# Performance work log

Hardware: AMD Instinct MI355X
Metric: run time of the kernel (lower is better)

The kernel has to match this reference:

```python
import jax, jax.numpy as jnp
import numpy as np

B, SQ, SK, D, N, H = 2, 2048, 2048, 1024, 16, 64
EPS = 1e-5


def setup_inputs() -> dict:
    key = jax.random.key(0)
    ks = jax.random.split(key, 8)
    inv_d = 1.0 / np.sqrt(D)
    inv_h = 1.0 / np.sqrt(H)
    # causal mask: True = masked (filled with -inf), matching torch.where(mask, IGNORE, attn)
    mask = jnp.triu(jnp.ones((SQ, SK), dtype=bool), k=1)
    return {
        "x_q": jax.random.normal(ks[0], (B, SQ, D), dtype=jnp.float32),
        "x_kv": jax.random.normal(ks[1], (B, SK, D), dtype=jnp.float32),
        "mask": mask,
        "W_Q": jax.random.normal(ks[2], (N, D, H), dtype=jnp.float32) * inv_d,
        "W_K": jax.random.normal(ks[3], (N, D, H), dtype=jnp.float32) * inv_d,
        "W_V": jax.random.normal(ks[4], (N, D, H), dtype=jnp.float32) * inv_d,
        "W_O": jax.random.normal(ks[5], (N, H, D), dtype=jnp.float32) * inv_h,
        "b_Q": jnp.zeros((N, H), dtype=jnp.float32),
        "b_K": jnp.zeros((N, H), dtype=jnp.float32),
        "b_V": jnp.zeros((N, H), dtype=jnp.float32),
        "b_O": jnp.zeros((D,), dtype=jnp.float32),
        "ln1_g": jnp.ones((H,), dtype=jnp.float32),
        "ln1_b": jnp.zeros((H,), dtype=jnp.float32),
        "ln2_g": jnp.ones((H,), dtype=jnp.float32),
        "ln2_b": jnp.zeros((H,), dtype=jnp.float32),
    }


def _layernorm(x, g, b):
    # LayerNorm over last dim (d_head), eps=1e-5, biased variance (torch default)
    m = jnp.mean(x, axis=-1, keepdims=True)
    v = jnp.mean(jnp.square(x - m), axis=-1, keepdims=True)
    return (x - m) * jax.lax.rsqrt(v + EPS) * g + b


def reference(x_q, x_kv, mask, W_Q, W_K, W_V, W_O, b_Q, b_K, b_V, b_O,
              ln1_g, ln1_b, ln2_g, ln2_b):
    q = jnp.einsum('bsd,ndh->bsnh', x_q, W_Q) + b_Q    # [B,SQ,N,H]
    k = jnp.einsum('bsd,ndh->bsnh', x_kv, W_K) + b_K   # [B,SK,N,H]
    v = jnp.einsum('bsd,ndh->bsnh', x_kv, W_V) + b_V   # [B,SK,N,H]
    q = _layernorm(q, ln1_g, ln1_b)
    k = _layernorm(k, ln2_g, ln2_b)
    # NOTE: no 1/sqrt(d_head) scaling, faithful to the source module
    attn = jnp.einsum('bqnh,bknh->bnqk', q, k)         # [B,N,SQ,SK]
    attn = jnp.where(mask, -jnp.inf, attn)
    probas = jax.nn.softmax(attn, axis=-1)
    z = jnp.einsum('bnqk,bknh->bqnh', probas, v)       # [B,SQ,N,H]
    out = jnp.einsum('bqnh,nhd->bqd', z, W_O) + b_O    # [B,SQ,D]
    return (out, k, v)
```

## Files before the change

kernel.cpp:

```cpp
#include <hip/hip_runtime.h>
#include <math.h>

namespace {
constexpr int kB  = 2;
constexpr int kS  = 2048;
constexpr int kD  = 1024;
constexpr int kN  = 16;
constexpr int kH  = 64;
constexpr int kBS = kB * kS;
constexpr int kNH = kN * kH;
}

typedef __bf16 bf16x4 __attribute__((ext_vector_type(4)));
typedef __bf16 bf16x8 __attribute__((ext_vector_type(8)));
typedef float  f32x4  __attribute__((ext_vector_type(4)));
typedef unsigned int u32x4 __attribute__((ext_vector_type(4)));

__device__ inline unsigned pkbf(float a, float b) {
  unsigned short ua = __builtin_bit_cast(unsigned short, (__bf16)a);
  unsigned short ub = __builtin_bit_cast(unsigned short, (__bf16)b);
  return (unsigned)ua | ((unsigned)ub << 16);
}

__global__ __launch_bounds__(256) void prep_all(
    const float* __restrict__ xq, const float* __restrict__ xkv,
    const float* __restrict__ WQ, const float* __restrict__ WK,
    const float* __restrict__ WV, const float* __restrict__ WO,
    __bf16* __restrict__ xqH, __bf16* __restrict__ xqL,
    __bf16* __restrict__ xkH, __bf16* __restrict__ xkL,
    __bf16* __restrict__ QH, __bf16* __restrict__ QL,
    __bf16* __restrict__ KHo, __bf16* __restrict__ KLo,
    __bf16* __restrict__ VH,
    __bf16* __restrict__ WOtH)
{
  const int bx = blockIdx.x;
  const int t = threadIdx.x;
  __shared__ float T[64][65];

  if (bx < 8192) {
    const float* in;
    __bf16 *oH, *oL;
    long long i4;
    if (bx < 4096) { in = xq;  oH = xqH; oL = xqL; i4 = (long long)bx * 256 + t; }
    else           { in = xkv; oH = xkH; oL = xkL; i4 = (long long)(bx - 4096) * 256 + t; }
    const float4 v = *(const float4*)(in + i4 * 4);
    const float x[4] = {v.x, v.y, v.z, v.w};
    bf16x4 hi, lo;
#pragma unroll
    for (int i = 0; i < 4; ++i) {
      const __bf16 h = (__bf16)x[i];
      hi[i] = h;
      lo[i] = (__bf16)(x[i] - (float)h);
    }
    *(bf16x4*)(oH + i4 * 4) = hi;
    *(bf16x4*)(oL + i4 * 4) = lo;
    return;
  }

  if (bx < 8960) {
    const int zz = bx - 8192;
    const int bxx = zz & 15;
    const int z   = zz >> 4;
    const int which = z >> 4;
    const bool wantLo = (which < 2);
    const float* __restrict__ in = (which == 0) ? WQ : (which == 1) ? WK : WV;
    __bf16* __restrict__ oH = (which == 0) ? QH : (which == 1) ? KHo : VH;
    __bf16* __restrict__ oL = (which == 0) ? QL : KLo;
    const int head = z & 15;
    const long long inB  = (long long)head * 65536 + (long long)(bxx * 64) * 64;
    const long long outB = (long long)head * 65536 + bxx * 64;
#pragma unroll
    for (int rr = 0; rr < 4; ++rr) {
      const int i = rr * 16 + (t >> 4);
      const int j = (t & 15) * 4;
      const float4 v = *(const float4*)(in + inB + (long long)i * 64 + j);
      T[i][j + 0] = v.x; T[i][j + 1] = v.y; T[i][j + 2] = v.z; T[i][j + 3] = v.w;
    }
    __syncthreads();
#pragma unroll
    for (int rr = 0; rr < 4; ++rr) {
      const int hh = rr * 16 + (t >> 4);
      const int kk = (t & 15) * 4;
      bf16x4 hi, lo;
#pragma unroll
      for (int m = 0; m < 4; ++m) {
        const float x = T[kk + m][hh];
        const __bf16 h = (__bf16)x;
        hi[m] = h;
        lo[m] = (__bf16)(x - (float)h);
      }
      *(bf16x4*)(oH + outB + (long long)hh * 1024 + kk) = hi;
      if (wantLo)
        *(bf16x4*)(oL + outB + (long long)hh * 1024 + kk) = lo;
    }
    return;
  }

  {
    const int zz = bx - 8960;
    const int bxx = zz & 15;
    const int byy = zz >> 4;
    const long long inB  = (long long)(bxx * 64) * 1024 + byy * 64;
    const long long outB = (long long)(byy * 64) * 1024 + bxx * 64;
#pragma unroll
    for (int rr = 0; rr < 4; ++rr) {
      const int i = rr * 16 + (t >> 4);
      const int j = (t & 15) * 4;
      const float4 v = *(const float4*)(WO + inB + (long long)i * 1024 + j);
      T[i][j + 0] = v.x; T[i][j + 1] = v.y; T[i][j + 2] = v.z; T[i][j + 3] = v.w;
    }
    __syncthreads();
#pragma unroll
    for (int rr = 0; rr < 4; ++rr) {
      const int hh = rr * 16 + (t >> 4);
      const int kk = (t & 15) * 4;
      bf16x4 hi;
#pragma unroll
      for (int m = 0; m < 4; ++m) hi[m] = (__bf16)T[kk + m][hh];
      *(bf16x4*)(WOtH + outB + (long long)hh * 1024 + kk) = hi;
    }
  }
}

__global__ __launch_bounds__(256) void qkv_gemm128v(
    const __bf16* __restrict__ xqH, const __bf16* __restrict__ xqL,
    const __bf16* __restrict__ xkH, const __bf16* __restrict__ xkL,
    const __bf16* __restrict__ WQH, const __bf16* __restrict__ WQL,
    const __bf16* __restrict__ WKH, const __bf16* __restrict__ WKL,
    const __bf16* __restrict__ WVH,
    const float* __restrict__ b_Q, const float* __restrict__ b_K,
    const float* __restrict__ b_V,
    const float* __restrict__ ln1g, const float* __restrict__ ln1b,
    const float* __restrict__ ln2g, const float* __restrict__ ln2b,
    float* __restrict__ out_k, float* __restrict__ out_v,
    __bf16* __restrict__ qH, __bf16* __restrict__ qL,
    __bf16* __restrict__ kHp, __bf16* __restrict__ kLp,
    __bf16* __restrict__ vT)
{
  const int mode = blockIdx.z;
  const int row0 = blockIdx.x * 128;
  const int ct   = blockIdx.y;
  const bool split = (mode < 2);

  __shared__ __align__(16) char SM[36864];
  char* const ABuf = SM;
  char* const BBuf = SM + 16384;

  const int t = threadIdx.x;
  const int lane = t & 63;
  const int w = t >> 6;
  const int l16 = lane & 15;
  const int quad = lane >> 4;
  const int mBase = (w & 1) * 64;
  const int nBase = (w >> 1) * 64;

  const __bf16* __restrict__ aHp = (mode == 0) ? xqH : xkH;
  const __bf16* __restrict__ aLq = split ? ((mode == 0) ? xqL : xkL) : aHp;
  const __bf16* __restrict__ bHp = (mode == 0) ? WQH : (mode == 1) ? WKH : WVH;
  const __bf16* __restrict__ bLq = split ? ((mode == 0) ? WQL : WKL) : bHp;

  f32x4 acc[4][4] = {};

  const int srow8 = lane >> 3;
  const int p     = lane & 7;
  const int sw2l  = (srow8 & 1) | ((srow8 & 2) << 1) | ((srow8 & 4) >> 1);
  const int u     = p ^ sw2l;
  const int ucol  = (u & 3) * 8;
  const __bf16* __restrict__ pA = (u < 4) ? aHp : aLq;
  const __bf16* __restrict__ pB = (u < 4) ? bHp : bLq;
  const long long gA0 = (long long)(row0 + w * 32 + srow8) * 1024 + ucol;
  const long long gB0 = (long long)(ct * 128 + w * 32 + srow8) * 1024 + ucol;
  char* const ABufW = ABuf + w * 4096;
  char* const BBufW = BBuf + w * 4096;

  const int r8  = l16 & 7;
  const int rs2 = (r8 & 1) | ((r8 & 2) << 1) | ((r8 & 4) >> 1);
  const int rof = (quad ^ rs2) << 4;

  auto COMPUTE = [&]() {
    bf16x8 ah[4], bh[4];
#pragma unroll
    for (int mt = 0; mt < 4; ++mt)
      ah[mt] = *(const bf16x8*)(ABuf + (mBase + mt * 16 + l16) * 128 + rof);
#pragma unroll
    for (int nt = 0; nt < 4; ++nt)
      bh[nt] = *(const bf16x8*)(BBuf + (nBase + nt * 16 + l16) * 128 + rof);
#pragma unroll
    for (int mt = 0; mt < 4; ++mt)
#pragma unroll
      for (int nt = 0; nt < 4; ++nt)
        acc[mt][nt] = __builtin_amdgcn_mfma_f32_16x16x32_bf16(ah[mt], bh[nt], acc[mt][nt], 0, 0, 0);
    if (split) {
      bf16x8 bl[4];
#pragma unroll
      for (int nt = 0; nt < 4; ++nt)
        bl[nt] = *(const bf16x8*)(BBuf + (nBase + nt * 16 + l16) * 128 + (rof ^ 64));
#pragma unroll
      for (int mt = 0; mt < 4; ++mt)
#pragma unroll
        for (int nt = 0; nt < 4; ++nt)
          acc[mt][nt] = __builtin_amdgcn_mfma_f32_16x16x32_bf16(ah[mt], bl[nt], acc[mt][nt], 0, 0, 0);
      bf16x8 al[4];
#pragma unroll
      for (int mt = 0; mt < 4; ++mt)
        al[mt] = *(const bf16x8*)(ABuf + (mBase + mt * 16 + l16) * 128 + (rof ^ 64));
#pragma unroll
      for (int mt = 0; mt < 4; ++mt)
#pragma unroll
        for (int nt = 0; nt < 4; ++nt)
          acc[mt][nt] = __builtin_amdgcn_mfma_f32_16x16x32_bf16(al[mt], bh[nt], acc[mt][nt], 0, 0, 0);
    }
  };

  for (int k0 = 0; k0 < 1024; k0 += 32) {
    if (k0) __syncthreads();
#pragma unroll
    for (int i = 0; i < 4; ++i) {
      __builtin_amdgcn_global_load_lds(
          (const __attribute__((address_space(1))) void*)(pA + gA0 + (long long)i * 8192 + k0),
          (__attribute__((address_space(3))) void*)(ABufW + i * 1024), 16, 0, 0);
      __builtin_amdgcn_global_load_lds(
          (const __attribute__((address_space(1))) void*)(pB + gB0 + (long long)i * 8192 + k0),
          (__attribute__((address_space(3))) void*)(BBufW + i * 1024), 16, 0, 0);
    }
    __syncthreads();
    COMPUTE();
  }

  const float* __restrict__ bias = (mode == 0) ? b_Q : (mode == 1) ? b_K : b_V;
  float bi[4];
#pragma unroll
  for (int nt = 0; nt < 4; ++nt) bi[nt] = bias[ct * 128 + nBase + nt * 16 + l16];

  if (mode <= 1) {
    const float* __restrict__ lg = (mode == 0) ? ln1g : ln2g;
    const float* __restrict__ lb = (mode == 0) ? ln1b : ln2b;
    float gg[4], bb[4];
#pragma unroll
    for (int nt = 0; nt < 4; ++nt) {
      gg[nt] = lg[nt * 16 + l16];
      bb[nt] = lb[nt * 16 + l16];
    }
#pragma unroll
    for (int mt = 0; mt < 4; ++mt)
#pragma unroll
      for (int r4 = 0; r4 < 4; ++r4) {
        float y[4];
#pragma unroll
        for (int nt = 0; nt < 4; ++nt) y[nt] = acc[mt][nt][r4] + bi[nt];
        float s = y[0] + y[1] + y[2] + y[3];
#pragma unroll
        for (int o = 8; o >= 1; o >>= 1) s += __shfl_xor(s, o);
        const float m = s * (1.0f / 64.0f);
        float vs = 0.0f;
#pragma unroll
        for (int nt = 0; nt < 4; ++nt) {
          const float d = y[nt] - m;
          vs += d * d;
        }
#pragma unroll
        for (int o = 8; o >= 1; o >>= 1) vs += __shfl_xor(vs, o);
        const float inv = rsqrtf(vs * (1.0f / 64.0f) + 1e-5f);
#pragma unroll
        for (int nt = 0; nt < 4; ++nt)
          acc[mt][nt][r4] = (y[nt] - m) * inv * gg[nt] + bb[nt];
      }
  } else {
#pragma unroll
    for (int mt = 0; mt < 4; ++mt)
#pragma unroll
      for (int nt = 0; nt < 4; ++nt)
#pragma unroll
        for (int r4 = 0; r4 < 4; ++r4) acc[mt][nt][r4] += bi[nt];
  }

#pragma unroll
  for (int mt = 0; mt < 4; ++mt)
#pragma unroll
    for (int r4 = 0; r4 < 4; ++r4) {
      const long long row = row0 + mBase + mt * 16 + quad * 4 + r4;
      const long long cb = row * 1024 + ct * 128 + nBase;
      if (mode == 0) {
#pragma unroll
        for (int nt = 0; nt < 4; ++nt) {
          const float x = acc[mt][nt][r4];
          const __bf16 h = (__bf16)x;
          qH[cb + nt * 16 + l16] = h;
          qL[cb + nt * 16 + l16] = (__bf16)(x - (float)h);
        }
      } else if (mode == 1) {
#pragma unroll
        for (int nt = 0; nt < 4; ++nt) {
          const float x = acc[mt][nt][r4];
          out_k[cb + nt * 16 + l16] = x;
          const __bf16 h = (__bf16)x;
          kHp[cb + nt * 16 + l16] = h;
          kLp[cb + nt * 16 + l16] = (__bf16)(x - (float)h);
        }
      } else {
#pragma unroll
        for (int nt = 0; nt < 4; ++nt)
          out_v[cb + nt * 16 + l16] = acc[mt][nt][r4];
      }
    }

  if (mode == 2) {
    __syncthreads();
    __bf16* TT = (__bf16*)SM + w * 4608;
#pragma unroll
    for (int mt = 0; mt < 4; ++mt)
#pragma unroll
      for (int nt = 0; nt < 4; ++nt)
#pragma unroll
        for (int r4 = 0; r4 < 4; ++r4)
          TT[(nt * 16 + l16) * 72 + mt * 16 + quad * 4 + r4] = (__bf16)acc[mt][nt][r4];
    __syncthreads();
    const int b = row0 >> 11;
    const int s0 = (row0 + mBase) & 2047;
    const int head = ct * 2 + (w >> 1);
#pragma unroll
    for (int rep = 0; rep < 8; ++rep) {
      const int h = rep * 8 + (lane >> 3);
      const int s8v = (lane & 7) * 8;
      const bf16x8 vv = *(const bf16x8*)&TT[h * 72 + s8v];
      const int a  = s8v >> 4;
      const int c0 = 32 * (a >> 1) + 8 * ((s8v >> 2) & 3) + 4 * (a & 1);
      __bf16* dst = vT + ((long long)((b * 16 + head) * 64 + h)) * 2048 + s0 + c0;
      const bf16x4 lo = __builtin_shufflevector(vv, vv, 0, 1, 2, 3);
      const bf16x4 hi = __builtin_shufflevector(vv, vv, 4, 5, 6, 7);
      *(bf16x4*)(dst)     = lo;
      *(bf16x4*)(dst + 8) = hi;
    }
  }
}

__global__ __launch_bounds__(256) void ogemm64p(
    const __bf16* __restrict__ zH, const __bf16* __restrict__ WOt,
    const float* __restrict__ b_O, float* __restrict__ out)
{
  const int row0 = blockIdx.x * 64;
  const int ct = blockIdx.y;
  __shared__ __align__(16) __bf16 AS2[2][64][40];
  __shared__ __align__(16) __bf16 BS2[2][128][40];
  const int t = threadIdx.x;
  const int lane = t & 63;
  const int w = t >> 6;
  const int l16 = lane & 15;
  const int quad = lane >> 4;
  const int nBase = w * 32;

  f32x4 acc[4][2] = {};
  const int arow = t >> 2, akh = (t & 3) * 8;
  const int brow = t >> 1, bkh = (t & 1) * 16;

  bf16x8 r0, r1, r2;
  auto loadT = [&](int k0) {
    r0 = *(const bf16x8*)(zH + (long long)(row0 + arow) * 1024 + k0 + akh);
    const long long gb = (long long)(ct * 128 + brow) * 1024 + k0 + bkh;
    r1 = *(const bf16x8*)(WOt + gb);
    r2 = *(const bf16x8*)(WOt + gb + 8);
  };
  loadT(0);
  *(bf16x8*)&AS2[0][arow][akh]     = r0;
  *(bf16x8*)&BS2[0][brow][bkh]     = r1;
  *(bf16x8*)&BS2[0][brow][bkh + 8] = r2;
  __syncthreads();

  for (int k0 = 0; k0 < 1024; k0 += 32) {
    const int cb = (k0 >> 5) & 1;
    const bool more = (k0 + 32 < 1024);
    if (more) loadT(k0 + 32);

    bf16x8 ah[4], bh[2];
#pragma unroll
    for (int mt = 0; mt < 4; ++mt)
      ah[mt] = *(const bf16x8*)&AS2[cb][mt * 16 + l16][quad * 8];
#pragma unroll
    for (int nt = 0; nt < 2; ++nt)
      bh[nt] = *(const bf16x8*)&BS2[cb][nBase + nt * 16 + l16][quad * 8];
#pragma unroll
    for (int mt = 0; mt < 4; ++mt)
#pragma unroll
      for (int nt = 0; nt < 2; ++nt)
        acc[mt][nt] = __builtin_amdgcn_mfma_f32_16x16x32_bf16(ah[mt], bh[nt], acc[mt][nt], 0, 0, 0);

    if (more) {
      const int nb = 1 - cb;
      *(bf16x8*)&AS2[nb][arow][akh]     = r0;
      *(bf16x8*)&BS2[nb][brow][bkh]     = r1;
      *(bf16x8*)&BS2[nb][brow][bkh + 8] = r2;
    }
    __syncthreads();
  }

#pragma unroll
  for (int mt = 0; mt < 4; ++mt)
#pragma unroll
    for (int r4 = 0; r4 < 4; ++r4) {
      const long long row = row0 + mt * 16 + quad * 4 + r4;
#pragma unroll
      for (int nt = 0; nt < 2; ++nt) {
        const int col = ct * 128 + nBase + nt * 16 + l16;
        out[row * 1024 + col] = acc[mt][nt][r4] + b_O[col];
      }
    }
}

__global__ __launch_bounds__(256, 2) void attn_mfma6(
    const __bf16* __restrict__ qHg, const __bf16* __restrict__ qLg,
    const __bf16* __restrict__ kHg, const __bf16* __restrict__ kLg,
    const __bf16* __restrict__ vTg,
    __bf16* __restrict__ zH)
{
  const int p = blockIdx.x;
  const int n = blockIdx.y;
  const int b = blockIdx.z;

  __shared__ __align__(16) char SM[49152];

  const int t = threadIdx.x;
  const int lane = t & 63;
  const int w = t >> 6;
  const int l16 = lane & 15;
  const int quad = lane >> 4;
  const int skey = t >> 2;
  const int sh16 = (t & 3) * 16;
  const int su   = sh16 >> 3;
  const int sx   = (skey & 7) << 4;
  const int rx   = (l16 & 7) << 4;

  bf16x8 rk0, rk1, rl0, rl1, rv0, rv1;
  auto storeKV = [&](int buf) {
    char* base = SM + buf * 8192 + skey * 128;
    *(bf16x8*)(base +         (((su    ) << 4) ^ sx)) = rk0;
    *(bf16x8*)(base +         (((su + 1) << 4) ^ sx)) = rk1;
    *(bf16x8*)(base + 16384 + (((su    ) << 4) ^ sx)) = rl0;
    *(bf16x8*)(base + 16384 + (((su + 1) << 4) ^ sx)) = rl1;
    *(bf16x8*)(base + 32768 + (((su    ) << 4) ^ sx)) = rv0;
    *(bf16x8*)(base + 32768 + (((su + 1) << 4) ^ sx)) = rv1;
  };

  for (int half = 0; half < 2; ++half) {
    const int qt = half ? p : (31 - p);
    const int q0 = qt * 64;

    bf16x8 Qh[2], Ql[2];
    {
      const long long qrow = (long long)(b * kS + q0 + w * 16 + l16) * 1024 + n * 64 + quad * 8;
      Qh[0] = *(const bf16x8*)(qHg + qrow);
      Qh[1] = *(const bf16x8*)(qHg + qrow + 32);
      Ql[0] = *(const bf16x8*)(qLg + qrow);
      Ql[1] = *(const bf16x8*)(qLg + qrow + 32);
    }

    f32x4 O[4] = {};
    float mrun = -3.0e38f, lrun = 0.0f;
    const int qg = q0 + w * 16 + l16;

    auto loadKV = [&](int k0) {
      const long long gk = (long long)(b * kS + k0 + skey) * 1024 + n * 64 + sh16;
      rk0 = *(const bf16x8*)(kHg + gk);
      rk1 = *(const bf16x8*)(kHg + gk + 8);
      rl0 = *(const bf16x8*)(kLg + gk);
      rl1 = *(const bf16x8*)(kLg + gk + 8);
      const long long gv = ((long long)(b * kN + n) * 64 + skey) * 2048 + k0 + sh16;
      rv0 = *(const bf16x8*)(vTg + gv);
      rv1 = *(const bf16x8*)(vTg + gv + 8);
    };

    loadKV(0);
    storeKV(0);
    __syncthreads();

    for (int kt = 0; kt <= qt; ++kt) {
      const int cb = kt & 1;
      const bool more = (kt < qt);
      if (more) loadKV((kt + 1) * 64);

      const char* KHb = SM + cb * 8192;
      const char* KLb = KHb + 16384;
      const char* VSb = KHb + 32768;

      f32x4 S[4] = {};
      __builtin_amdgcn_s_setprio(1);
#pragma unroll
      for (int kc = 0; kc < 4; ++kc) {
        const int ro = (kc * 16 + l16) * 128;
        const bf16x8 kh0 = *(const bf16x8*)(KHb + ro + (((quad    ) << 4) ^ rx));
        const bf16x8 kh1 = *(const bf16x8*)(KHb + ro + (((quad + 4) << 4) ^ rx));
        const bf16x8 kl0 = *(const bf16x8*)(KLb + ro + (((quad    ) << 4) ^ rx));
        const bf16x8 kl1 = *(const bf16x8*)(KLb + ro + (((quad + 4) << 4) ^ rx));
        S[kc] = __builtin_amdgcn_mfma_f32_16x16x32_bf16(kh0, Qh[0], S[kc], 0, 0, 0);
        S[kc] = __builtin_amdgcn_mfma_f32_16x16x32_bf16(kh1, Qh[1], S[kc], 0, 0, 0);
        S[kc] = __builtin_amdgcn_mfma_f32_16x16x32_bf16(kl0, Qh[0], S[kc], 0, 0, 0);
        S[kc] = __builtin_amdgcn_mfma_f32_16x16x32_bf16(kl1, Qh[1], S[kc], 0, 0, 0);
        S[kc] = __builtin_amdgcn_mfma_f32_16x16x32_bf16(kh0, Ql[0], S[kc], 0, 0, 0);
        S[kc] = __builtin_amdgcn_mfma_f32_16x16x32_bf16(kh1, Ql[1], S[kc], 0, 0, 0);
      }
      __builtin_amdgcn_s_setprio(0);

      if (kt == qt) {
#pragma unroll
        for (int kc = 0; kc < 4; ++kc) {
          const int key = q0 + kc * 16 + quad * 4;
#pragma unroll
          for (int r = 0; r < 4; ++r)
            if (key + r > qg) S[kc][r] = -3.0e38f;
        }
      }

      float pm = fmaxf(fmaxf(S[0][0], S[0][1]), fmaxf(S[0][2], S[0][3]));
      pm = fmaxf(pm, fmaxf(fmaxf(S[1][0], S[1][1]), fmaxf(S[1][2], S[1][3])));
      pm = fmaxf(pm, fmaxf(fmaxf(S[2][0], S[2][1]), fmaxf(S[2][2], S[2][3])));
      pm = fmaxf(pm, fmaxf(fmaxf(S[3][0], S[3][1]), fmaxf(S[3][2], S[3][3])));
      pm = fmaxf(pm, __shfl_xor(pm, 16));
      pm = fmaxf(pm, __shfl_xor(pm, 32));

      const bool upd = __any(pm > mrun + 8.0f);
      const float mref = upd ? fmaxf(mrun, pm) : mrun;
      float ls = 0.0f;
#pragma unroll
      for (int kc = 0; kc < 4; ++kc)
#pragma unroll
        for (int r = 0; r < 4; ++r) {
          const float pe = __expf(S[kc][r] - mref);
          S[kc][r] = pe;
          ls += pe;
        }
      ls += __shfl_xor(ls, 16);
      ls += __shfl_xor(ls, 32);

      if (upd) {
        const float alpha = __expf(mrun - mref);
        lrun = lrun * alpha + ls;
        float aB[4];
#pragma unroll
        for (int r = 0; r < 4; ++r)
          aB[r] = __shfl(alpha, (lane & 48) | (quad * 4 + r));
#pragma unroll
        for (int hc = 0; hc < 4; ++hc)
#pragma unroll
          for (int r = 0; r < 4; ++r) O[hc][r] *= aB[r];
        mrun = mref;
      } else {
        lrun += ls;
      }

      u32x4 pw0, pw1;
      pw0[0] = pkbf(S[0][0], S[0][1]); pw0[1] = pkbf(S[0][2], S[0][3]);
      pw0[2] = pkbf(S[1][0], S[1][1]); pw0[3] = pkbf(S[1][2], S[1][3]);
      pw1[0] = pkbf(S[2][0], S[2][1]); pw1[1] = pkbf(S[2][2], S[2][3]);
      pw1[2] = pkbf(S[3][0], S[3][1]); pw1[3] = pkbf(S[3][2], S[3][3]);
      const bf16x8 Pa0 = __builtin_bit_cast(bf16x8, pw0);
      const bf16x8 Pa1 = __builtin_bit_cast(bf16x8, pw1);

      __builtin_amdgcn_s_setprio(1);
#pragma unroll
      for (int hc = 0; hc < 4; ++hc) {
        const int ro = (hc * 16 + l16) * 128;
        const bf16x8 vb0 = *(const bf16x8*)(VSb + ro + (((quad    ) << 4) ^ rx));
        const bf16x8 vb1 = *(const bf16x8*)(VSb + ro + (((quad + 4) << 4) ^ rx));
        O[hc] = __builtin_amdgcn_mfma_f32_16x16x32_bf16(Pa0, vb0, O[hc], 0, 0, 0);
        O[hc] = __builtin_amdgcn_mfma_f32_16x16x32_bf16(Pa1, vb1, O[hc], 0, 0, 0);
      }
      __builtin_amdgcn_s_setprio(0);

      if (more) storeKV(1 - cb);
      __syncthreads();
    }

    float linv[4];
#pragma unroll
    for (int r = 0; r < 4; ++r)
      linv[r] = 1.0f / __shfl(lrun, (lane & 48) | (quad * 4 + r));
#pragma unroll
    for (int r = 0; r < 4; ++r) {
      const long long zrow = (long long)(b * kS + q0 + w * 16 + quad * 4 + r) * 1024 + n * 64;
#pragma unroll
      for (int hc = 0; hc < 4; ++hc)
        zH[zrow + hc * 16 + l16] = (__bf16)(O[hc][r] * linv[r]);
    }
  }
}

__global__ __launch_bounds__(256) void sgemm64(
    const float* __restrict__ A, int lda,
    const float* __restrict__ Bbase, long long bStride, int colMul, int ldb,
    float* __restrict__ C, int ldc,
    const float* __restrict__ bias, int K)
{
  const int row0 = blockIdx.x * 64;
  const int ct = blockIdx.y;
  const float* __restrict__ Bp = Bbase + (long long)ct * bStride;
  const int col0B = ct * colMul;
  const int col0C = ct * 64;
  __shared__ float As[16][68];
  __shared__ float Bs[16][68];
  const int t = threadIdx.x;
  const int ty = t >> 4;
  const int tx = t & 15;
  float acc[4][4] = {};
  for (int k0 = 0; k0 < K; k0 += 16) {
    {
      const int r = t >> 2;
      const int kk = (t & 3) * 4;
      const float4 a4 = *(const float4*)(A + (long long)(row0 + r) * lda + k0 + kk);
      As[kk + 0][r] = a4.x; As[kk + 1][r] = a4.y; As[kk + 2][r] = a4.z; As[kk + 3][r] = a4.w;
    }
    {
      const int kk = t >> 4;
      const int c = (t & 15) * 4;
      *(float4*)&Bs[kk][c] = *(const float4*)(Bp + (long long)(k0 + kk) * ldb + col0B + c);
    }
    __syncthreads();
#pragma unroll
    for (int kk = 0; kk < 16; ++kk) {
      const float4 a4 = *(const float4*)&As[kk][ty * 4];
      const float4 b4 = *(const float4*)&Bs[kk][tx * 4];
      const float av[4] = {a4.x, a4.y, a4.z, a4.w};
      const float bv[4] = {b4.x, b4.y, b4.z, b4.w};
#pragma unroll
      for (int i = 0; i < 4; ++i)
#pragma unroll
        for (int j = 0; j < 4; ++j)
          acc[i][j] = fmaf(av[i], bv[j], acc[i][j]);
    }
    __syncthreads();
  }
#pragma unroll
  for (int i = 0; i < 4; ++i) {
    const int r = row0 + ty * 4 + i;
    float4 o;
    o.x = acc[i][0] + bias[col0C + tx * 4 + 0];
    o.y = acc[i][1] + bias[col0C + tx * 4 + 1];
    o.z = acc[i][2] + bias[col0C + tx * 4 + 2];
    o.w = acc[i][3] + bias[col0C + tx * 4 + 3];
    *(float4*)(C + (long long)r * ldc + col0C + tx * 4) = o;
  }
}

__global__ __launch_bounds__(256) void ln64(
    float* __restrict__ X, const float* __restrict__ g,
    const float* __restrict__ bta, int nrows)
{
  const int row = blockIdx.x * 4 + (threadIdx.x >> 6);
  const int lane = threadIdx.x & 63;
  if (row >= nrows) return;
  const float x = X[(long long)row * 64 + lane];
  float s = x;
#pragma unroll
  for (int o = 32; o >= 1; o >>= 1) s += __shfl_xor(s, o);
  const float m = s * (1.0f / 64.0f);
  const float d = x - m;
  float vs = d * d;
#pragma unroll
  for (int o = 32; o >= 1; o >>= 1) vs += __shfl_xor(vs, o);
  const float inv = rsqrtf(vs * (1.0f / 64.0f) + 1e-5f);
  X[(long long)row * 64 + lane] = d * inv * g[lane] + bta[lane];
}

__global__ __launch_bounds__(256) void attn_mfma(
    const float* __restrict__ Q, const float* __restrict__ Kg,
    const float* __restrict__ Vg, float* __restrict__ Z)
{
  const int qt = (gridDim.x - 1) - blockIdx.x;
  const int n = blockIdx.y;
  const int b = blockIdx.z;
  const int q0 = qt * 64;
  __shared__ __bf16 KH[64][72];
  __shared__ __bf16 KL[64][72];
  __shared__ __bf16 VS[64][72];
  const int t = threadIdx.x;
  const int lane = t & 63;
  const int w = t >> 6;
  const int l16 = lane & 15;
  const int quad = lane >> 4;
  bf16x8 Qh[2], Ql[2];
  {
    const long long qrow = ((long long)(b * kS + q0 + w * 16 + l16)) * kNH + n * kH + quad * 8;
#pragma unroll
    for (int c = 0; c < 2; ++c) {
      const float4 a = *(const float4*)(Q + qrow + c * 32);
      const float4 bq = *(const float4*)(Q + qrow + c * 32 + 4);
      const float x[8] = {a.x, a.y, a.z, a.w, bq.x, bq.y, bq.z, bq.w};
#pragma unroll
      for (int i = 0; i < 8; ++i) {
        const __bf16 h = (__bf16)x[i];
        Qh[c][i] = h;
        Ql[c][i] = (__bf16)(x[i] - (float)h);
      }
    }
  }
  f32x4 O[4] = {};
  float mrow[4] = {-3.0e38f, -3.0e38f, -3.0e38f, -3.0e38f};
  float lrow[4] = {};
  for (int kt = 0; kt <= qt; ++kt) {
    const int k0 = kt * 64;
    __syncthreads();
#pragma unroll
    for (int rep = 0; rep < 4; ++rep) {
      {
        const int row = rep * 16 + (t >> 4);
        const int h4 = (t & 15) * 4;
        const float4 k4 = *(const float4*)(Kg + ((long long)(b * kS + k0 + row)) * kNH + n * kH + h4);
        const float x[4] = {k4.x, k4.y, k4.z, k4.w};
        bf16x4 hi, lo;
#pragma unroll
        for (int i = 0; i < 4; ++i) {
          const __bf16 h = (__bf16)x[i];
          hi[i] = h;
          lo[i] = (__bf16)(x[i] - (float)h);
        }
        *(bf16x4*)&KH[row][h4] = hi;
        *(bf16x4*)&KL[row][h4] = lo;
      }
      {
        const int key = rep * 16 + (t & 15);
        const int h4 = (t >> 4) * 4;
        const float4 v4 = *(const float4*)(Vg + ((long long)(b * kS + k0 + key)) * kNH + n * kH + h4);
        VS[h4 + 0][key] = (__bf16)v4.x;
        VS[h4 + 1][key] = (__bf16)v4.y;
        VS[h4 + 2][key] = (__bf16)v4.z;
        VS[h4 + 3][key] = (__bf16)v4.w;
      }
    }
    __syncthreads();
    f32x4 S[4] = {};
#pragma unroll
    for (int kc = 0; kc < 4; ++kc) {
      const int row = kc * 16 + l16;
      const bf16x8 kh0 = *(const bf16x8*)&KH[row][quad * 8];
      const bf16x8 kh1 = *(const bf16x8*)&KH[row][32 + quad * 8];
      const bf16x8 kl0 = *(const bf16x8*)&KL[row][quad * 8];
      const bf16x8 kl1 = *(const bf16x8*)&KL[row][32 + quad * 8];
      S[kc] = __builtin_amdgcn_mfma_f32_16x16x32_bf16(Qh[0], kh0, S[kc], 0, 0, 0);
      S[kc] = __builtin_amdgcn_mfma_f32_16x16x32_bf16(Qh[1], kh1, S[kc], 0, 0, 0);
      S[kc] = __builtin_amdgcn_mfma_f32_16x16x32_bf16(Qh[0], kl0, S[kc], 0, 0, 0);
      S[kc] = __builtin_amdgcn_mfma_f32_16x16x32_bf16(Qh[1], kl1, S[kc], 0, 0, 0);
      S[kc] = __builtin_amdgcn_mfma_f32_16x16x32_bf16(Ql[0], kh0, S[kc], 0, 0, 0);
      S[kc] = __builtin_amdgcn_mfma_f32_16x16x32_bf16(Ql[1], kh1, S[kc], 0, 0, 0);
    }
    if (kt == qt) {
#pragma unroll
      for (int kc = 0; kc < 4; ++kc) {
        const int key = k0 + kc * 16 + l16;
#pragma unroll
        for (int r = 0; r < 4; ++r) {
          const int q = q0 + w * 16 + quad * 4 + r;
          if (key > q) S[kc][r] = -3.0e38f;
        }
      }
    }
#pragma unroll
    for (int r = 0; r < 4; ++r) {
      float mt = fmaxf(fmaxf(S[0][r], S[1][r]), fmaxf(S[2][r], S[3][r]));
#pragma unroll
      for (int o = 8; o >= 1; o >>= 1) mt = fmaxf(mt, __shfl_xor(mt, o));
      const float mnew = fmaxf(mrow[r], mt);
      const float alpha = __expf(mrow[r] - mnew);
      mrow[r] = mnew;
      float ls = 0.0f;
#pragma unroll
      for (int kc = 0; kc < 4; ++kc) {
        const float pe = __expf(S[kc][r] - mnew);
        S[kc][r] = pe;
        ls += pe;
      }
#pragma unroll
      for (int o = 8; o >= 1; o >>= 1) ls += __shfl_xor(ls, o);
      lrow[r] = lrow[r] * alpha + ls;
#pragma unroll
      for (int hc = 0; hc < 4; ++hc) O[hc][r] *= alpha;
    }
    __syncthreads();
    __bf16(*Ps)[72] = KL;
#pragma unroll
    for (int kc = 0; kc < 4; ++kc)
#pragma unroll
      for (int r = 0; r < 4; ++r)
        Ps[w * 16 + quad * 4 + r][kc * 16 + l16] = (__bf16)S[kc][r];
    bf16x8 Pa[2];
#pragma unroll
    for (int c = 0; c < 2; ++c)
      Pa[c] = *(const bf16x8*)&Ps[w * 16 + l16][c * 32 + quad * 8];
#pragma unroll
    for (int hc = 0; hc < 4; ++hc) {
      const int hrow = hc * 16 + l16;
      const bf16x8 vb0 = *(const bf16x8*)&VS[hrow][quad * 8];
      const bf16x8 vb1 = *(const bf16x8*)&VS[hrow][32 + quad * 8];
      O[hc] = __builtin_amdgcn_mfma_f32_16x16x32_bf16(Pa[0], vb0, O[hc], 0, 0, 0);
      O[hc] = __builtin_amdgcn_mfma_f32_16x16x32_bf16(Pa[1], vb1, O[hc], 0, 0, 0);
    }
  }
#pragma unroll
  for (int r = 0; r < 4; ++r) {
    const float inv = 1.0f / lrow[r];
    const long long zrow = ((long long)(b * kS + q0 + w * 16 + quad * 4 + r)) * kNH + n * kH;
#pragma unroll
    for (int hc = 0; hc < 4; ++hc)
      Z[zrow + hc * 16 + l16] = O[hc][r] * inv;
  }
}

extern "C" void kernel_launch(void* const* d_in, const int* in_sizes, int n_in,
                              void* d_out, int out_size, void* d_ws, size_t ws_size,
                              hipStream_t stream)
{
  const float* x_q   = (const float*)d_in[0];
  const float* x_kv  = (const float*)d_in[1];
  const float* W_Q   = (const float*)d_in[3];
  const float* W_K   = (const float*)d_in[4];
  const float* W_V   = (const float*)d_in[5];
  const float* W_O   = (const float*)d_in[6];
  const float* b_Q   = (const float*)d_in[7];
  const float* b_K   = (const float*)d_in[8];
  const float* b_V   = (const float*)d_in[9];
  const float* b_O   = (const float*)d_in[10];
  const float* ln1_g = (const float*)d_in[11];
  const float* ln1_b = (const float*)d_in[12];
  const float* ln2_g = (const float*)d_in[13];
  const float* ln2_b = (const float*)d_in[14];

  float* out_o = (float*)d_out;
  float* out_k = out_o + 4194304;
  float* out_v = out_o + 8388608;

  const dim3 blk(256);

  if (ws_size >= (72ull << 20)) {
    char* W = (char*)d_ws;
    __bf16* xqH = (__bf16*)(W);
    __bf16* xqL = xqH + 4194304;
    __bf16* xkH = (__bf16*)(W + (16ull << 20));
    __bf16* xkL = xkH + 4194304;
    __bf16* wp  = (__bf16*)(W + (32ull << 20));
    __bf16 *WtQH = wp,            *WtQL = wp + 1048576;
    __bf16 *WtKH = wp + 2097152,  *WtKL = wp + 3145728;
    __bf16 *WtVH = wp + 4194304;
    __bf16 *WOtH = wp + 6291456;
    __bf16* kHp = (__bf16*)(W + (48ull << 20));
    __bf16* kLp = kHp + 4194304;
    __bf16* vT  = (__bf16*)(W + (64ull << 20));
    __bf16* zH = xqH;
    __bf16* qH = (__bf16*)out_o;
    __bf16* qL = qH + 4194304;

    hipLaunchKernelGGL(prep_all, dim3(9216), blk, 0, stream,
                       x_q, x_kv, W_Q, W_K, W_V, W_O,
                       xqH, xqL, xkH, xkL,
                       WtQH, WtQL, WtKH, WtKL, WtVH, WOtH);

    hipLaunchKernelGGL(qkv_gemm128v, dim3(32, 8, 3), blk, 0, stream,
                       xqH, xqL, xkH, xkL,
                       WtQH, WtQL, WtKH, WtKL, WtVH,
                       b_Q, b_K, b_V, ln1_g, ln1_b, ln2_g, ln2_b,
                       out_k, out_v, qH, qL, kHp, kLp, vT);

    hipLaunchKernelGGL(attn_mfma6, dim3(16, 16, 2), blk, 0, stream,
                       qH, qL, kHp, kLp, vT, zH);

    hipLaunchKernelGGL(ogemm64p, dim3(64, 8), blk, 0, stream,
                       zH, WOtH, b_O, out_o);
  } else {
    float* ws_q = out_o;
    float* ws_z = (float*)d_ws;
    const dim3 gproj(kBS / 64, kN);
    hipLaunchKernelGGL(sgemm64, gproj, blk, 0, stream,
                       x_q, kD, W_Q, (long long)kD * kH, 0, kH, ws_q, kNH, b_Q, kD);
    hipLaunchKernelGGL(sgemm64, gproj, blk, 0, stream,
                       x_kv, kD, W_K, (long long)kD * kH, 0, kH, out_k, kNH, b_K, kD);
    hipLaunchKernelGGL(sgemm64, gproj, blk, 0, stream,
                       x_kv, kD, W_V, (long long)kD * kH, 0, kH, out_v, kNH, b_V, kD);
    const int nrows = kBS * kN;
    hipLaunchKernelGGL(ln64, dim3(nrows / 4), blk, 0, stream, ws_q, ln1_g, ln1_b, nrows);
    hipLaunchKernelGGL(ln64, dim3(nrows / 4), blk, 0, stream, out_k, ln2_g, ln2_b, nrows);
    hipLaunchKernelGGL(attn_mfma, dim3(kS / 64, kN, kB), blk, 0, stream,
                       ws_q, out_k, out_v, ws_z);
    hipLaunchKernelGGL(sgemm64, dim3(kBS / 64, kD / 64), blk, 0, stream,
                       ws_z, kNH, W_O, 0LL, 64, kD, out_o, kD, b_O, kD);
  }
}
```

Measured before the change: 295.4 us.

## Enlarge attention query tile to 128 rows with two 16-row slices per wave

The attention kernel now gives each wave two 16-row query slices (128 query rows per block), so every K/V tile staged in shared memory feeds twice as many MFMAs. This halves the total K/V global traffic and shared-memory reads per unit of compute. The grid drops to 8x16x2 blocks with launch bounds of one block per SIMD, so occupancy and parallelism fall and register pressure from the doubled accumulators and softmax state rises. Causal masking now covers the last two key tiles of each query block.

After: 304.5 us. +3.1%, slower.

```diff
diff --git a/kernel.cpp b/kernel.cpp
--- a/kernel.cpp
+++ b/kernel.cpp
@@ -406,7 +406,7 @@
     }
 }
 
-__global__ __launch_bounds__(256, 2) void attn_mfma6(
+__global__ __launch_bounds__(256, 1) void attn_mfma7(
     const __bf16* __restrict__ qHg, const __bf16* __restrict__ qLg,
     const __bf16* __restrict__ kHg, const __bf16* __restrict__ kLg,
     const __bf16* __restrict__ vTg,
@@ -441,21 +441,28 @@
   };
 
   for (int half = 0; half < 2; ++half) {
-    const int qt = half ? p : (31 - p);
-    const int q0 = qt * 64;
-
-    bf16x8 Qh[2], Ql[2];
+    const int qt = half ? p : (15 - p);
+    const int q0 = qt * 128;
+    const int nkt = 2 * qt + 2;
+
+    bf16x8 QhA[2], QlA[2], QhB[2], QlB[2];
     {
-      const long long qrow = (long long)(b * kS + q0 + w * 16 + l16) * 1024 + n * 64 + quad * 8;
-      Qh[0] = *(const bf16x8*)(qHg + qrow);
-      Qh[1] = *(const bf16x8*)(qHg + qrow + 32);
-      Ql[0] = *(const bf16x8*)(qLg + qrow);
-      Ql[1] = *(const bf16x8*)(qLg + qrow + 32);
-    }
-
-    f32x4 O[4] = {};
-    float mrun = -3.0e38f, lrun = 0.0f;
-    const int qg = q0 + w * 16 + l16;
+      const long long qrowA = (long long)(b * kS + q0 + w * 32 + l16) * 1024 + n * 64 + quad * 8;
+      QhA[0] = *(const bf16x8*)(qHg + qrowA);
+      QhA[1] = *(const bf16x8*)(qHg + qrowA + 32);
+      QlA[0] = *(const bf16x8*)(qLg + qrowA);
+      QlA[1] = *(const bf16x8*)(qLg + qrowA + 32);
+      const long long qrowB = qrowA + 16 * 1024;
+      QhB[0] = *(const bf16x8*)(qHg + qrowB);
+      QhB[1] = *(const bf16x8*)(qHg + qrowB + 32);
+      QlB[0] = *(const bf16x8*)(qLg + qrowB);
+      QlB[1] = *(const bf16x8*)(qLg + qrowB + 32);
+    }
+
+    f32x4 OA[4] = {}, OB[4] = {};
+    float mA = -3.0e38f, lA = 0.0f, mB = -3.0e38f, lB = 0.0f;
+    const int qa = q0 + w * 32 + l16;
+    const int qb = qa + 16;
 
     auto loadKV = [&](int k0) {
       const long long gk = (long long)(b * kS + k0 + skey) * 1024 + n * 64 + sh16;
@@ -472,16 +479,16 @@
     storeKV(0);
     __syncthreads();
 
-    for (int kt = 0; kt <= qt; ++kt) {
+    for (int kt = 0; kt < nkt; ++kt) {
       const int cb = kt & 1;
-      const bool more = (kt < qt);
+      const bool more = (kt + 1 < nkt);
       if (more) loadKV((kt + 1) * 64);
 
       const char* KHb = SM + cb * 8192;
       const char* KLb = KHb + 16384;
       const char* VSb = KHb + 32768;
 
-      f32x4 S[4] = {};
+      f32x4 SA[4] = {}, SB[4] = {};
       __builtin_amdgcn_s_setprio(1);
 #pragma unroll
       for (int kc = 0; kc < 4; ++kc) {
@@ -490,69 +497,117 @@
         const bf16x8 kh1 = *(const bf16x8*)(KHb + ro + (((quad + 4) << 4) ^ rx));
         const bf16x8 kl0 = *(const bf16x8*)(KLb + ro + (((quad    ) << 4) ^ rx));
         const bf16x8 kl1 = *(const bf16x8*)(KLb + ro + (((quad + 4) << 4) ^ rx));
-        S[kc] = __builtin_amdgcn_mfma_f32_16x16x32_bf16(kh0, Qh[0], S[kc], 0, 0, 0);
-        S[kc] = __builtin_amdgcn_mfma_f32_16x16x32_bf16(kh1, Qh[1], S[kc], 0, 0, 0);
-        S[kc] = __builtin_amdgcn_mfma_f32_16x16x32_bf16(kl0, Qh[0], S[kc], 0, 0, 0);
-        S[kc] = __builtin_amdgcn_mfma_f32_16x16x32_bf16(kl1, Qh[1], S[kc], 0, 0, 0);
-        S[kc] = __builtin_amdgcn_mfma_f32_16x16x32_bf16(kh0, Ql[0], S[kc], 0, 0, 0);
-        S[kc] = __builtin_amdgcn_mfma_f32_16x16x32_bf16(kh1, Ql[1], S[kc], 0, 0, 0);
+        SA[kc] = __builtin_amdgcn_mfma_f32_16x16x32_bf16(kh0, QhA[0], SA[kc], 0, 0, 0);
+        SA[kc] = __builtin_amdgcn_mfma_f32_16x16x32_bf16(kh1, QhA[1], SA[kc], 0, 0, 0);
+        SA[kc] = __builtin_amdgcn_mfma_f32_16x16x32_bf16(kl0, QhA[0], SA[kc], 0, 0, 0);
+        SA[kc] = __builtin_amdgcn_mfma_f32_16x16x32_bf16(kl1, QhA[1], SA[kc], 0, 0, 0);
+        SA[kc] = __builtin_amdgcn_mfma_f32_16x16x32_bf16(kh0, QlA[0], SA[kc], 0, 0, 0);
+        SA[kc] = __builtin_amdgcn_mfma_f32_16x16x32_bf16(kh1, QlA[1], SA[kc], 0, 0, 0);
+        SB[kc] = __builtin_amdgcn_mfma_f32_16x16x32_bf16(kh0, QhB[0], SB[kc], 0, 0, 0);
+        SB[kc] = __builtin_amdgcn_mfma_f32_16x16x32_bf16(kh1, QhB[1], SB[kc], 0, 0, 0);
+        SB[kc] = __builtin_amdgcn_mfma_f32_16x16x32_bf16(kl0, QhB[0], SB[kc], 0, 0, 0);
+        SB[kc] = __builtin_amdgcn_mfma_f32_16x16x32_bf16(kl1, QhB[1], SB[kc], 0, 0, 0);
+        SB[kc] = __builtin_amdgcn_mfma_f32_16x16x32_bf16(kh0, QlB[0], SB[kc], 0, 0, 0);
+        SB[kc] = __builtin_amdgcn_mfma_f32_16x16x32_bf16(kh1, QlB[1], SB[kc], 0, 0, 0);
       }
       __builtin_amdgcn_s_setprio(0);
 
-      if (kt == qt) {
+      if (kt >= 2 * qt) {
 #pragma unroll
         for (int kc = 0; kc < 4; ++kc) {
-          const int key = q0 + kc * 16 + quad * 4;
-#pragma unroll
-          for (int r = 0; r < 4; ++r)
-            if (key + r > qg) S[kc][r] = -3.0e38f;
+          const int key = kt * 64 + kc * 16 + quad * 4;
+#pragma unroll
+          for (int r = 0; r < 4; ++r) {
+            if (key + r > qa) SA[kc][r] = -3.0e38f;
+            if (key + r > qb) SB[kc][r] = -3.0e38f;
+          }
         }
       }
 
-      float pm = fmaxf(fmaxf(S[0][0], S[0][1]), fmaxf(S[0][2], S[0][3]));
-      pm = fmaxf(pm, fmaxf(fmaxf(S[1][0], S[1][1]), fmaxf(S[1][2], S[1][3])));
-      pm = fmaxf(pm, fmaxf(fmaxf(S[2][0], S[2][1]), fmaxf(S[2][2], S[2][3])));
-      pm = fmaxf(pm, fmaxf(fmaxf(S[3][0], S[3][1]), fmaxf(S[3][2], S[3][3])));
-      pm = fmaxf(pm, __shfl_xor(pm, 16));
-      pm = fmaxf(pm, __shfl_xor(pm, 32));
-
-      const bool upd = __any(pm > mrun + 8.0f);
-      const float mref = upd ? fmaxf(mrun, pm) : mrun;
-      float ls = 0.0f;
+      float pmA = fmaxf(fmaxf(SA[0][0], SA[0][1]), fmaxf(SA[0][2], SA[0][3]));
+      pmA = fmaxf(pmA, fmaxf(fmaxf(SA[1][0], SA[1][1]), fmaxf(SA[1][2], SA[1][3])));
+      pmA = fmaxf(pmA, fmaxf(fmaxf(SA[2][0], SA[2][1]), fmaxf(SA[2][2], SA[2][3])));
+      pmA = fmaxf(pmA, fmaxf(fmaxf(SA[3][0], SA[3][1]), fmaxf(SA[3][2], SA[3][3])));
+      pmA = fmaxf(pmA, __shfl_xor(pmA, 16));
+      pmA = fmaxf(pmA, __shfl_xor(pmA, 32));
+      float pmB = fmaxf(fmaxf(SB[0][0], SB[0][1]), fmaxf(SB[0][2], SB[0][3]));
+      pmB = fmaxf(pmB, fmaxf(fmaxf(SB[1][0], SB[1][1]), fmaxf(SB[1][2], SB[1][3])));
+      pmB = fmaxf(pmB, fmaxf(fmaxf(SB[2][0], SB[2][1]), fmaxf(SB[2][2], SB[2][3])));
+      pmB = fmaxf(pmB, fmaxf(fmaxf(SB[3][0], SB[3][1]), fmaxf(SB[3][2], SB[3][3])));
+      pmB = fmaxf(pmB, __shfl_xor(pmB, 16));
+      pmB = fmaxf(pmB, __shfl_xor(pmB, 32));
+
+      const bool updA = __any(pmA > mA + 8.0f);
+      const float mrefA = updA ? fmaxf(mA, pmA) : mA;
+      float lsA = 0.0f;
 #pragma unroll
       for (int kc = 0; kc < 4; ++kc)
 #pragma unroll
         for (int r = 0; r < 4; ++r) {
-          const float pe = __expf(S[kc][r] - mref);
-          S[kc][r] = pe;
-          ls += pe;
+          const float pe = __expf(SA[kc][r] - mrefA);
+          SA[kc][r] = pe;
+          lsA += pe;
         }
-      ls += __shfl_xor(ls, 16);
-      ls += __shfl_xor(ls, 32);
-
-      if (upd) {
-        const float alpha = __expf(mrun - mref);
-        lrun = lrun * alpha + ls;
-        float aB[4];
+      lsA += __shfl_xor(lsA, 16);
+      lsA += __shfl_xor(lsA, 32);
+      if (updA) {
+        const float alpha = __expf(mA - mrefA);
+        lA = lA * alpha + lsA;
+        float aB4[4];
 #pragma unroll
         for (int r = 0; r < 4; ++r)
-          aB[r] = __shfl(alpha, (lane & 48) | (quad * 4 + r));
+          aB4[r] = __shfl(alpha, (lane & 48) | (quad * 4 + r));
 #pragma unroll
         for (int hc = 0; hc < 4; ++hc)
 #pragma unroll
-          for (int r = 0; r < 4; ++r) O[hc][r] *= aB[r];
-        mrun = mref;
+          for (int r = 0; r < 4; ++r) OA[hc][r] *= aB4[r];
+        mA = mrefA;
       } else {
-        lrun += ls;
+        lA += lsA;
+      }
+
+      const bool updB = __any(pmB > mB + 8.0f);
+      const float mrefB = updB ? fmaxf(mB, pmB) : mB;
+      float lsB = 0.0f;
+#pragma unroll
+      for (int kc = 0; kc < 4; ++kc)
+#pragma unroll
+        for (int r = 0; r < 4; ++r) {
+          const float pe = __expf(SB[kc][r] - mrefB);
+          SB[kc][r] = pe;
+          lsB += pe;
+        }
+      lsB += __shfl_xor(lsB, 16);
+      lsB += __shfl_xor(lsB, 32);
+      if (updB) {
+        const float alpha = __expf(mB - mrefB);
+        lB = lB * alpha + lsB;
+        float aB4[4];
+#pragma unroll
+        for (int r = 0; r < 4; ++r)
+          aB4[r] = __shfl(alpha, (lane & 48) | (quad * 4 + r));
+#pragma unroll
+        for (int hc = 0; hc < 4; ++hc)
+#pragma unroll
+          for (int r = 0; r < 4; ++r) OB[hc][r] *= aB4[r];
+        mB = mrefB;
+      } else {
+        lB += lsB;
       }
 
       u32x4 pw0, pw1;
-      pw0[0] = pkbf(S[0][0], S[0][1]); pw0[1] = pkbf(S[0][2], S[0][3]);
-      pw0[2] = pkbf(S[1][0], S[1][1]); pw0[3] = pkbf(S[1][2], S[1][3]);
-      pw1[0] = pkbf(S[2][0], S[2][1]); pw1[1] = pkbf(S[2][2], S[2][3]);
-      pw1[2] = pkbf(S[3][0], S[3][1]); pw1[3] = pkbf(S[3][2], S[3][3]);
-      const bf16x8 Pa0 = __builtin_bit_cast(bf16x8, pw0);
-      const bf16x8 Pa1 = __builtin_bit_cast(bf16x8, pw1);
+      pw0[0] = pkbf(SA[0][0], SA[0][1]); pw0[1] = pkbf(SA[0][2], SA[0][3]);
+      pw0[2] = pkbf(SA[1][0], SA[1][1]); pw0[3] = pkbf(SA[1][2], SA[1][3]);
+      pw1[0] = pkbf(SA[2][0], SA[2][1]); pw1[1] = pkbf(SA[2][2], SA[2][3]);
+      pw1[2] = pkbf(SA[3][0], SA[3][1]); pw1[3] = pkbf(SA[3][2], SA[3][3]);
+      const bf16x8 Pa0A = __builtin_bit_cast(bf16x8, pw0);
+      const bf16x8 Pa1A = __builtin_bit_cast(bf16x8, pw1);
+      pw0[0] = pkbf(SB[0][0], SB[0][1]); pw0[1] = pkbf(SB[0][2], SB[0][3]);
+      pw0[2] = pkbf(SB[1][0], SB[1][1]); pw0[3] = pkbf(SB[1][2], SB[1][3]);
+      pw1[0] = pkbf(SB[2][0], SB[2][1]); pw1[1] = pkbf(SB[2][2], SB[2][3]);
+      pw1[2] = pkbf(SB[3][0], SB[3][1]); pw1[3] = pkbf(SB[3][2], SB[3][3]);
+      const bf16x8 Pa0B = __builtin_bit_cast(bf16x8, pw0);
+      const bf16x8 Pa1B = __builtin_bit_cast(bf16x8, pw1);
 
       __builtin_amdgcn_s_setprio(1);
 #pragma unroll
@@ -560,8 +615,10 @@
         const int ro = (hc * 16 + l16) * 128;
         const bf16x8 vb0 = *(const bf16x8*)(VSb + ro + (((quad    ) << 4) ^ rx));
         const bf16x8 vb1 = *(const bf16x8*)(VSb + ro + (((quad + 4) << 4) ^ rx));
-        O[hc] = __builtin_amdgcn_mfma_f32_16x16x32_bf16(Pa0, vb0, O[hc], 0, 0, 0);
-        O[hc] = __builtin_amdgcn_mfma_f32_16x16x32_bf16(Pa1, vb1, O[hc], 0, 0, 0);
+        OA[hc] = __builtin_amdgcn_mfma_f32_16x16x32_bf16(Pa0A, vb0, OA[hc], 0, 0, 0);
+        OA[hc] = __builtin_amdgcn_mfma_f32_16x16x32_bf16(Pa1A, vb1, OA[hc], 0, 0, 0);
+        OB[hc] = __builtin_amdgcn_mfma_f32_16x16x32_bf16(Pa0B, vb0, OB[hc], 0, 0, 0);
+        OB[hc] = __builtin_amdgcn_mfma_f32_16x16x32_bf16(Pa1B, vb1, OB[hc], 0, 0, 0);
       }
       __builtin_amdgcn_s_setprio(0);
 
@@ -569,16 +626,22 @@
       __syncthreads();
     }
 
-    float linv[4];
-#pragma unroll
-    for (int r = 0; r < 4; ++r)
-      linv[r] = 1.0f / __shfl(lrun, (lane & 48) | (quad * 4 + r));
+    float linvA[4], linvB[4];
 #pragma unroll
     for (int r = 0; r < 4; ++r) {
-      const long long zrow = (long long)(b * kS + q0 + w * 16 + quad * 4 + r) * 1024 + n * 64;
+      linvA[r] = 1.0f / __shfl(lA, (lane & 48) | (quad * 4 + r));
+      linvB[r] = 1.0f / __shfl(lB, (lane & 48) | (quad * 4 + r));
+    }
+#pragma unroll
+    for (int r = 0; r < 4; ++r) {
+      const long long zrowA = (long long)(b * kS + q0 + w * 32 + quad * 4 + r) * 1024 + n * 64;
 #pragma unroll
       for (int hc = 0; hc < 4; ++hc)
-        zH[zrow + hc * 16 + l16] = (__bf16)(O[hc][r] * linv[r]);
+        zH[zrowA + hc * 16 + l16] = (__bf16)(OA[hc][r] * linvA[r]);
+      const long long zrowB = zrowA + 16 * 1024;
+#pragma unroll
+      for (int hc = 0; hc < 4; ++hc)
+        zH[zrowB + hc * 16 + l16] = (__bf16)(OB[hc][r] * linvB[r]);
     }
   }
 }
@@ -856,7 +919,7 @@
                        b_Q, b_K, b_V, ln1_g, ln1_b, ln2_g, ln2_b,
                        out_k, out_v, qH, qL, kHp, kLp, vT);
 
-    hipLaunchKernelGGL(attn_mfma6, dim3(16, 16, 2), blk, 0, stream,
+    hipLaunchKernelGGL(attn_mfma7, dim3(8, 16, 2), blk, 0, stream,
                        qH, qL, kHp, kLp, vT, zH);
 
     hipLaunchKernelGGL(ogemm64p, dim3(64, 8), blk, 0, stream,
```
